# Performance work log

Hardware: AMD Instinct MI355X
Metric: run time of the kernel (lower is better)

## Reference

```python
import jax, jax.numpy as jnp
import numpy as np

N_WIRES = 10
DIM = 1 << N_WIRES          # 1024 amplitudes per token state
HIDDEN = 64                 # number of Pauli-Z-string measurements (= hidden_dim)
B, T = 8, 2048

# ops[k] = Z-string on qubits in bitmask (k+1): <psi|Z_mask|psi> = sum_i |psi_i|^2 * (-1)^popcount(i & mask)
_masks = np.arange(1, HIDDEN + 1, dtype=np.int64)
_ii = np.arange(DIM, dtype=np.int64)
_pc = (((_ii[None, :] & _masks[:, None])[..., None] >> np.arange(N_WIRES)) & 1).sum(-1)
SIGNS = jnp.asarray(1.0 - 2.0 * (_pc % 2), dtype=jnp.float32)   # (HIDDEN, DIM)

CNOT = jnp.array([[1, 0, 0, 0], [0, 1, 0, 0], [0, 0, 0, 1], [0, 0, 1, 0]], dtype=jnp.complex64)

def _rx(theta):
    c = jnp.cos(theta / 2).astype(jnp.complex64)
    s = jnp.sin(theta / 2).astype(jnp.complex64)
    return jnp.stack([jnp.stack([c, -1j * s]), jnp.stack([-1j * s, c])])

def _ry(theta):
    c = jnp.cos(theta / 2).astype(jnp.complex64)
    s = jnp.sin(theta / 2).astype(jnp.complex64)
    return jnp.stack([jnp.stack([c, -s]), jnp.stack([s, c])])

def _apply_1q(psi, g, j, n):
    # qubit 0 is the most-significant bit of the state index (matches expand_operator bit order)
    left, right = 1 << j, 1 << (n - 1 - j)
    p = psi.reshape(-1, left, 2, right)
    p = jnp.einsum('ab,mlbr->mlar', g, p)
    return p.reshape(-1, 1 << n)

def _apply_2q(psi, g, q0, q1, n):
    p = psi.reshape((-1,) + (2,) * n)
    p = jnp.moveaxis(p, (1 + q0, 1 + q1), (1, 2))
    p = jnp.einsum('abcd,mcd...->mab...', g.reshape(2, 2, 2, 2), p)
    p = jnp.moveaxis(p, (1, 2), (1 + q0, 1 + q1))
    return p.reshape(-1, 1 << n)

def _forward(x, rx0, ry0, ry1):
    n, dim = N_WIRES, DIM
    Bb, Tt, C = x.shape
    M = Bb * Tt
    # AmplitudeEncoder: zero-pad features to 2^n and L2-normalize
    psi = jnp.zeros((M, dim), jnp.complex64).at[:, :C].set(x.reshape(M, C).astype(jnp.complex64))
    nrm = jnp.sqrt(jnp.sum(psi.real**2 + psi.imag**2, axis=1, keepdims=True))
    psi = psi / nrm.astype(jnp.complex64)
    # U_total = (prod_j RY1_j) (prod_j CNOT_{j,(j+1)%n}) (prod_j RY0_j RX0_j), applied to psi.
    # Applying the gate sequence directly to the state == matmul with the expanded U_total.
    rx0_d = jax.lax.stop_gradient(rx0)  # original detaches RX params via .item()
    for j in range(n):
        psi = _apply_1q(psi, _rx(rx0_d[j]), j, n)
        psi = _apply_1q(psi, _ry(ry0[j]), j, n)
    for j in range(n):
        psi = _apply_2q(psi, CNOT, j, (j + 1) % n, n)
    for j in range(n):
        psi = _apply_1q(psi, _ry(ry1[j]), j, n)
    probs = psi.real**2 + psi.imag**2            # (M, DIM)
    out = probs @ SIGNS.T                        # (M, HIDDEN) Pauli-Z-string expectations
    return out.reshape(Bb, Tt, HIDDEN).astype(jnp.float32)

def setup_inputs():
    key = jax.random.key(0)
    k1, k2, k3, k4 = jax.random.split(key, 4)
    two_pi = 2.0 * float(np.pi)
    return {
        'x': jax.random.normal(k1, (B, T, HIDDEN), dtype=jnp.float32),
        'rx0': jax.random.uniform(k2, (N_WIRES,), dtype=jnp.float32, maxval=two_pi),
        'ry0': jax.random.uniform(k3, (N_WIRES,), dtype=jnp.float32, maxval=two_pi),
        'ry1': jax.random.uniform(k4, (N_WIRES,), dtype=jnp.float32, maxval=two_pi),
    }

def reference(x, rx0, ry0, ry1):
    return _forward(x, rx0, ry0, ry1)
```

## Files before the change

kernel.cpp:

```cpp
#include <hip/hip_runtime.h>

typedef __bf16 v8bf __attribute__((ext_vector_type(8)));
typedef float v4f __attribute__((ext_vector_type(4)));
typedef unsigned short u16x8 __attribute__((ext_vector_type(8)));

__device__ __forceinline__ unsigned short f2bf(float f) {
    unsigned int u = __float_as_uint(f);
    u += 0x7FFFu + ((u >> 16) & 1u);
    return (unsigned short)(u >> 16);
}

__device__ __forceinline__ v8bf ld_bf8(const unsigned short* p) {
    u16x8 r = *(const u16x8*)p;
    return __builtin_bit_cast(v8bf, r);
}

__device__ __forceinline__ float hw_cos(float h) {
    float r = h * 0.15915494309189535f, o;
    asm("v_cos_f32 %0, %1" : "=v"(o) : "v"(r));
    return o;
}
__device__ __forceinline__ float hw_sin(float h) {
    float r = h * 0.15915494309189535f, o;
    asm("v_sin_f32 %0, %1" : "=v"(o) : "v"(r));
    return o;
}

__global__ __launch_bounds__(64, 2) void build_V(
        const float* __restrict__ rx0, const float* __restrict__ ry0,
        const float* __restrict__ ry1,
        unsigned short* __restrict__ Vre, unsigned short* __restrict__ Vim)
{
    const int c = blockIdx.x;
    const int lane = threadIdx.x;

    float c1[10], s1[10];
    #pragma unroll
    for (int j = 0; j < 10; ++j) {
        float h = 0.5f * ry1[j];
        c1[j] = hw_cos(h); s1[j] = hw_sin(h);
    }

    int kk[16];
    #pragma unroll
    for (int q = 0; q < 16; ++q) {
        int k = lane + (q << 6);
        #pragma unroll
        for (int jj = 9; jj >= 0; --jj) {
            int cb = 9 - jj, tb = 9 - ((jj + 1) % 10);
            k ^= ((k >> cb) & 1) << tb;
        }
        kk[q] = k;
    }

    float ar[16], ai[16];
    #pragma unroll
    for (int q = 0; q < 16; ++q) { ar[q] = 1.f; ai[q] = 0.f; }

    #pragma unroll
    for (int j = 0; j < 10; ++j) {
        float hx = 0.5f * rx0[j], hy = 0.5f * ry0[j];
        float cx = hw_cos(hx), sx = hw_sin(hx), cy = hw_cos(hy), sy = hw_sin(hy);
        int cb = (c >> (9 - j)) & 1;
        float g0r = cb ? (-sy * cx) : (cy * cx);
        float g0i = cb ? (-cy * sx) : (sy * sx);
        float g1r = cb ? (cy * cx)  : (sy * cx);
        float g1i = cb ? (-sy * sx) : (-cy * sx);
        int p = 9 - j;
        #pragma unroll
        for (int q = 0; q < 16; ++q) {
            int kb = (kk[q] >> p) & 1;
            float fr = kb ? g1r : g0r;
            float fi = kb ? g1i : g0i;
            float nr = ar[q] * fr - ai[q] * fi;
            float ni = ar[q] * fi + ai[q] * fr;
            ar[q] = nr; ai[q] = ni;
        }
    }

    #pragma unroll
    for (int b = 0; b < 4; ++b) {
        float cy = c1[3 - b], sy = s1[3 - b];
        #pragma unroll
        for (int q = 0; q < 16; ++q) {
            if (q & (1 << b)) continue;
            int q2 = q | (1 << b);
            float A_r = ar[q], A_i = ai[q], B_r = ar[q2], B_i = ai[q2];
            ar[q]  = cy * A_r - sy * B_r;  ai[q]  = cy * A_i - sy * B_i;
            ar[q2] = sy * A_r + cy * B_r;  ai[q2] = sy * A_i + cy * B_i;
        }
    }
    #pragma unroll
    for (int p = 5; p >= 0; --p) {
        float cy = c1[9 - p], sy = s1[9 - p];
        int hi = (lane >> p) & 1;
        #pragma unroll
        for (int q = 0; q < 16; ++q) {
            float orr = __shfl_xor(ar[q], 1 << p);
            float oii = __shfl_xor(ai[q], 1 << p);
            ar[q] = hi ? (sy * orr + cy * ar[q]) : (cy * ar[q] - sy * orr);
            ai[q] = hi ? (sy * oii + cy * ai[q]) : (cy * ai[q] - sy * oii);
        }
    }

    #pragma unroll
    for (int q = 0; q < 16; ++q) {
        int i = lane + (q << 6);
        Vre[i * 64 + c] = f2bf(ar[q]);
        Vim[i * 64 + c] = f2bf(ai[q]);
    }
}

#define MFMA16(a, b, c) __builtin_amdgcn_mfma_f32_16x16x32_bf16(a, b, c, 0, 0, 0)

#define ISSUE(s, c) do {                                                     \
    _Pragma("unroll")                                                        \
    for (int _nb = 0; _nb < 4; ++_nb) {                                      \
        s[_nb*2+0] = ld_bf8(vb + (size_t)(c) * 4096 + _nb * 1024);           \
        s[_nb*2+1] = ld_bf8(vb + (size_t)(c) * 4096 + _nb * 1024 + 32);      \
    }                                                                        \
    __builtin_amdgcn_sched_barrier(0);                                       \
    } while (0)

#define COMP(s, q) do {                                                      \
    _Pragma("unroll")                                                        \
    for (int _nb = 0; _nb < 4; ++_nb) {                                      \
        v4f _z = (v4f){0.f, 0.f, 0.f, 0.f};                                  \
        v4f _r = MFMA16(a0, s[_nb*2+0], _z);                                 \
        _r     = MFMA16(a1, s[_nb*2+1], _r);                                 \
        _Pragma("unroll")                                                    \
        for (int _rr = 0; _rr < 4; ++_rr)                                    \
            q[_nb][_rr] += _r[_rr] * _r[_rr];                                \
    } } while (0)

#define GROUP(b) do {                                                        \
    if ((b) + 2 < 32) ISSUE(sC, (b) + 2);  COMP(sA, qE);                     \
    if ((b) + 3 < 32) ISSUE(sD, (b) + 3);  COMP(sB, qO);                     \
    if ((b) + 4 < 32) ISSUE(sA, (b) + 4);  COMP(sC, qE);                     \
    if ((b) + 5 < 32) ISSUE(sB, (b) + 5);  COMP(sD, qO);                     \
    } while (0)

__global__ __launch_bounds__(64) void qsa_fused(
        const float* __restrict__ x,
        const unsigned short* __restrict__ VS,
        float* __restrict__ out)
{
    const int l = threadIdx.x;
    const int l15 = l & 15, lh = l >> 4;
    const int tb = blockIdx.x * 16;

    const float* xrow = x + (size_t)(tb + l15) * 64;
    float4 v0 = *(const float4*)(xrow + lh * 8);
    float4 v1 = *(const float4*)(xrow + lh * 8 + 4);
    float4 v2 = *(const float4*)(xrow + 32 + lh * 8);
    float4 v3 = *(const float4*)(xrow + 32 + lh * 8 + 4);
    float ss = v0.x*v0.x + v0.y*v0.y + v0.z*v0.z + v0.w*v0.w
             + v1.x*v1.x + v1.y*v1.y + v1.z*v1.z + v1.w*v1.w
             + v2.x*v2.x + v2.y*v2.y + v2.z*v2.z + v2.w*v2.w
             + v3.x*v3.x + v3.y*v3.y + v3.z*v3.z + v3.w*v3.w;
    ss += __shfl_xor(ss, 16);
    ss += __shfl_xor(ss, 32);
    float rn = rsqrtf(ss);
    u16x8 ua0, ua1;
    ua0[0]=f2bf(v0.x*rn); ua0[1]=f2bf(v0.y*rn); ua0[2]=f2bf(v0.z*rn); ua0[3]=f2bf(v0.w*rn);
    ua0[4]=f2bf(v1.x*rn); ua0[5]=f2bf(v1.y*rn); ua0[6]=f2bf(v1.z*rn); ua0[7]=f2bf(v1.w*rn);
    ua1[0]=f2bf(v2.x*rn); ua1[1]=f2bf(v2.y*rn); ua1[2]=f2bf(v2.z*rn); ua1[3]=f2bf(v2.w*rn);
    ua1[4]=f2bf(v3.x*rn); ua1[5]=f2bf(v3.y*rn); ua1[6]=f2bf(v3.z*rn); ua1[7]=f2bf(v3.w*rn);
    const v8bf a0 = __builtin_bit_cast(v8bf, ua0);
    const v8bf a1 = __builtin_bit_cast(v8bf, ua1);

    const unsigned short* vb = VS + (size_t)l15 * 64 + lh * 8;

    float qE[4][4], qO[4][4];
    #pragma unroll
    for (int nb = 0; nb < 4; ++nb)
        #pragma unroll
        for (int rr = 0; rr < 4; ++rr) { qE[nb][rr] = 0.f; qO[nb][rr] = 0.f; }

    v8bf sA[8], sB[8], sC[8], sD[8];

    ISSUE(sA, 0);
    ISSUE(sB, 1);
    GROUP(0);  GROUP(4);  GROUP(8);  GROUP(12);
    GROUP(16); GROUP(20); GROUP(24); GROUP(28);

    #pragma unroll
    for (int rr = 0; rr < 4; ++rr) {
        float w8[8];
        #pragma unroll
        for (int nb = 0; nb < 4; ++nb) { w8[nb] = qE[nb][rr]; w8[4 + nb] = qO[nb][rr]; }

        #pragma unroll
        for (int i = 0; i < 4; ++i) {
            float u = w8[i], v = w8[i + 4];
            w8[i] = u + v; w8[i + 4] = u - v;
        }
        #pragma unroll
        for (int g = 0; g < 8; g += 4)
            #pragma unroll
            for (int i = 0; i < 2; ++i) {
                float u = w8[g + i], v = w8[g + i + 2];
                w8[g + i] = u + v; w8[g + i + 2] = u - v;
            }
        #pragma unroll
        for (int g = 0; g < 8; g += 2) {
            float u = w8[g], v = w8[g + 1];
            w8[g] = u + v; w8[g + 1] = u - v;
        }
        #pragma unroll
        for (int st = 1; st <= 8; st <<= 1) {
            #pragma unroll
            for (int k = 0; k < 8; ++k) {
                float o = __shfl_xor(w8[k], st);
                w8[k] = (l15 & st) ? (o - w8[k]) : (w8[k] + o);
            }
        }
        float* orow = out + (size_t)(tb + lh * 4 + rr) * 64;
        #pragma unroll
        for (int nb = 0; nb < 4; ++nb)
            if (nb != 0 || l15 != 0) orow[nb * 16 + l15 - 1] = w8[nb];
        if (l15 == 0) orow[63] = w8[4];
    }
}

extern "C" void kernel_launch(void* const* d_in, const int* in_sizes, int n_in,
                              void* d_out, int out_size, void* d_ws, size_t ws_size,
                              hipStream_t stream) {
    const float* x   = (const float*)d_in[0];
    const float* rx0 = (const float*)d_in[1];
    const float* ry0 = (const float*)d_in[2];
    const float* ry1 = (const float*)d_in[3];
    float* out = (float*)d_out;

    unsigned short* Vre = (unsigned short*)d_ws;
    unsigned short* Vim = Vre + 1024 * 64;

    const int M = in_sizes[0] / 64;

    build_V<<<64, 64, 0, stream>>>(rx0, ry0, ry1, Vre, Vim);
    qsa_fused<<<M / 16, 64, 0, stream>>>(x, Vre, out);
}
```

Baseline: 106.9 us.

## Split V chunk loop across two waves per block with LDS reduction

Each block now runs two wavefronts that each process half of the 32 V chunks (16 each), rather than one wave walking all 32. The second wave writes its partial squared accumulators to shared memory, and after a barrier the first wave adds them and performs the Walsh-Hadamard output transform. The software pipeline drops from four staging buffers to two to lower register use per wave. This roughly halves the serial MFMA and load chain per token tile and adds more waves per block, at the cost of an LDS round trip, a barrier, and the second wave sitting idle during the epilogue.

```diff
diff --git a/kernel.cpp b/kernel.cpp
--- a/kernel.cpp
+++ b/kernel.cpp
@@ -116,8 +116,8 @@
 #define ISSUE(s, c) do {                                                     \
     _Pragma("unroll")                                                        \
     for (int _nb = 0; _nb < 4; ++_nb) {                                      \
-        s[_nb*2+0] = ld_bf8(vb + (size_t)(c) * 4096 + _nb * 1024);           \
-        s[_nb*2+1] = ld_bf8(vb + (size_t)(c) * 4096 + _nb * 1024 + 32);      \
+        s[_nb*2+0] = ld_bf8(vbh + (size_t)(c) * 4096 + _nb * 1024);          \
+        s[_nb*2+1] = ld_bf8(vbh + (size_t)(c) * 4096 + _nb * 1024 + 32);     \
     }                                                                        \
     __builtin_amdgcn_sched_barrier(0);                                       \
     } while (0)
@@ -133,19 +133,21 @@
             q[_nb][_rr] += _r[_rr] * _r[_rr];                                \
     } } while (0)
 
-#define GROUP(b) do {                                                        \
-    if ((b) + 2 < 32) ISSUE(sC, (b) + 2);  COMP(sA, qE);                     \
-    if ((b) + 3 < 32) ISSUE(sD, (b) + 3);  COMP(sB, qO);                     \
-    if ((b) + 4 < 32) ISSUE(sA, (b) + 4);  COMP(sC, qE);                     \
-    if ((b) + 5 < 32) ISSUE(sB, (b) + 5);  COMP(sD, qO);                     \
+#define GR(b) do {                                                           \
+    if ((b) + 1 < 16) ISSUE(sB, (b) + 1);  COMP(sA, qE);                     \
+    if ((b) + 2 < 16) ISSUE(sA, (b) + 2);  COMP(sB, qO);                     \
     } while (0)
 
-__global__ __launch_bounds__(64) void qsa_fused(
+__global__ __launch_bounds__(128, 2) void qsa_fused(
         const float* __restrict__ x,
         const unsigned short* __restrict__ VS,
         float* __restrict__ out)
 {
-    const int l = threadIdx.x;
+    __shared__ float part[64][33];
+
+    const int tid = threadIdx.x;
+    const int w = tid >> 6;
+    const int l = tid & 63;
     const int l15 = l & 15, lh = l >> 4;
     const int tb = blockIdx.x * 16;
 
@@ -169,7 +171,7 @@
     const v8bf a0 = __builtin_bit_cast(v8bf, ua0);
     const v8bf a1 = __builtin_bit_cast(v8bf, ua1);
 
-    const unsigned short* vb = VS + (size_t)l15 * 64 + lh * 8;
+    const unsigned short* vbh = VS + (size_t)w * 16 * 4096 + (size_t)l15 * 64 + lh * 8;
 
     float qE[4][4], qO[4][4];
     #pragma unroll
@@ -177,49 +179,67 @@
         #pragma unroll
         for (int rr = 0; rr < 4; ++rr) { qE[nb][rr] = 0.f; qO[nb][rr] = 0.f; }
 
-    v8bf sA[8], sB[8], sC[8], sD[8];
+    v8bf sA[8], sB[8];
 
     ISSUE(sA, 0);
-    ISSUE(sB, 1);
-    GROUP(0);  GROUP(4);  GROUP(8);  GROUP(12);
-    GROUP(16); GROUP(20); GROUP(24); GROUP(28);
-
-    #pragma unroll
-    for (int rr = 0; rr < 4; ++rr) {
-        float w8[8];
-        #pragma unroll
-        for (int nb = 0; nb < 4; ++nb) { w8[nb] = qE[nb][rr]; w8[4 + nb] = qO[nb][rr]; }
-
-        #pragma unroll
-        for (int i = 0; i < 4; ++i) {
-            float u = w8[i], v = w8[i + 4];
-            w8[i] = u + v; w8[i + 4] = u - v;
-        }
-        #pragma unroll
-        for (int g = 0; g < 8; g += 4)
-            #pragma unroll
-            for (int i = 0; i < 2; ++i) {
-                float u = w8[g + i], v = w8[g + i + 2];
-                w8[g + i] = u + v; w8[g + i + 2] = u - v;
-            }
-        #pragma unroll
-        for (int g = 0; g < 8; g += 2) {
-            float u = w8[g], v = w8[g + 1];
-            w8[g] = u + v; w8[g + 1] = u - v;
-        }
-        #pragma unroll
-        for (int st = 1; st <= 8; st <<= 1) {
-            #pragma unroll
-            for (int k = 0; k < 8; ++k) {
-                float o = __shfl_xor(w8[k], st);
-                w8[k] = (l15 & st) ? (o - w8[k]) : (w8[k] + o);
-            }
-        }
-        float* orow = out + (size_t)(tb + lh * 4 + rr) * 64;
+    GR(0); GR(2); GR(4); GR(6); GR(8); GR(10); GR(12); GR(14);
+
+    if (w == 1) {
         #pragma unroll
         for (int nb = 0; nb < 4; ++nb)
-            if (nb != 0 || l15 != 0) orow[nb * 16 + l15 - 1] = w8[nb];
-        if (l15 == 0) orow[63] = w8[4];
+            #pragma unroll
+            for (int rr = 0; rr < 4; ++rr) {
+                part[l][nb * 4 + rr]      = qE[nb][rr];
+                part[l][16 + nb * 4 + rr] = qO[nb][rr];
+            }
+    }
+    __syncthreads();
+    if (w == 0) {
+        #pragma unroll
+        for (int nb = 0; nb < 4; ++nb)
+            #pragma unroll
+            for (int rr = 0; rr < 4; ++rr) {
+                qE[nb][rr] += part[l][nb * 4 + rr];
+                qO[nb][rr] += part[l][16 + nb * 4 + rr];
+            }
+
+        #pragma unroll
+        for (int rr = 0; rr < 4; ++rr) {
+            float w8[8];
+            #pragma unroll
+            for (int nb = 0; nb < 4; ++nb) { w8[nb] = qE[nb][rr]; w8[4 + nb] = qO[nb][rr]; }
+
+            #pragma unroll
+            for (int i = 0; i < 4; ++i) {
+                float u = w8[i], v = w8[i + 4];
+                w8[i] = u + v; w8[i + 4] = u - v;
+            }
+            #pragma unroll
+            for (int g = 0; g < 8; g += 4)
+                #pragma unroll
+                for (int i = 0; i < 2; ++i) {
+                    float u = w8[g + i], v = w8[g + i + 2];
+                    w8[g + i] = u + v; w8[g + i + 2] = u - v;
+                }
+            #pragma unroll
+            for (int g = 0; g < 8; g += 2) {
+                float u = w8[g], v = w8[g + 1];
+                w8[g] = u + v; w8[g + 1] = u - v;
+            }
+            #pragma unroll
+            for (int st = 1; st <= 8; st <<= 1) {
+                #pragma unroll
+                for (int k = 0; k < 8; ++k) {
+                    float o = __shfl_xor(w8[k], st);
+                    w8[k] = (l15 & st) ? (o - w8[k]) : (w8[k] + o);
+                }
+            }
+            float* orow = out + (size_t)(tb + lh * 4 + rr) * 64;
+            #pragma unroll
+            for (int nb = 0; nb < 4; ++nb)
+                if (nb != 0 || l15 != 0) orow[nb * 16 + l15 - 1] = w8[nb];
+            if (l15 == 0) orow[63] = w8[4];
+        }
     }
 }
 
@@ -238,5 +258,5 @@
     const int M = in_sizes[0] / 64;
 
     build_V<<<64, 64, 0, stream>>>(rx0, ry0, ry1, Vre, Vim);
-    qsa_fused<<<M / 16, 64, 0, stream>>>(x, Vre, out);
-}
+    qsa_fused<<<M / 16, 128, 0, stream>>>(x, Vre, out);
+}
```

Result: slower. 111.1 us (+4.0%).

## Use two-wave blocks with double buffering and pointer-increment loads

Applied to the files above, without the earlier changes.

Blocks now hold two waves of 64 threads, each handling its own 16 tokens, with launch bounds asking for 3 blocks per CU. The four-deep register prefetch ring (sA..sD) is cut to two buffers, and per-chunk address arithmetic is replaced by a running pointer. The goal is to free registers so more waves fit per CU and so latency is hidden by occupancy rather than deep prefetch. In exchange, each wave has less load lookahead of its own, which could expose memory latency if occupancy does not rise enough.

```diff
diff --git a/kernel.cpp b/kernel.cpp
--- a/kernel.cpp
+++ b/kernel.cpp
@@ -113,12 +113,14 @@
 
 #define MFMA16(a, b, c) __builtin_amdgcn_mfma_f32_16x16x32_bf16(a, b, c, 0, 0, 0)
 
-#define ISSUE(s, c) do {                                                     \
-    _Pragma("unroll")                                                        \
-    for (int _nb = 0; _nb < 4; ++_nb) {                                      \
-        s[_nb*2+0] = ld_bf8(vb + (size_t)(c) * 4096 + _nb * 1024);           \
-        s[_nb*2+1] = ld_bf8(vb + (size_t)(c) * 4096 + _nb * 1024 + 32);      \
-    }                                                                        \
+#define ISSUE(s) do {                                                        \
+    const unsigned short* _b0 = vp;                                          \
+    const unsigned short* _b1 = vp + 2048;                                   \
+    s[0] = ld_bf8(_b0);        s[1] = ld_bf8(_b0 + 32);                      \
+    s[2] = ld_bf8(_b0 + 1024); s[3] = ld_bf8(_b0 + 1056);                    \
+    s[4] = ld_bf8(_b1);        s[5] = ld_bf8(_b1 + 32);                      \
+    s[6] = ld_bf8(_b1 + 1024); s[7] = ld_bf8(_b1 + 1056);                    \
+    vp += 4096;                                                              \
     __builtin_amdgcn_sched_barrier(0);                                       \
     } while (0)
 
@@ -133,21 +135,18 @@
             q[_nb][_rr] += _r[_rr] * _r[_rr];                                \
     } } while (0)
 
-#define GROUP(b) do {                                                        \
-    if ((b) + 2 < 32) ISSUE(sC, (b) + 2);  COMP(sA, qE);                     \
-    if ((b) + 3 < 32) ISSUE(sD, (b) + 3);  COMP(sB, qO);                     \
-    if ((b) + 4 < 32) ISSUE(sA, (b) + 4);  COMP(sC, qE);                     \
-    if ((b) + 5 < 32) ISSUE(sB, (b) + 5);  COMP(sD, qO);                     \
-    } while (0)
-
-__global__ __launch_bounds__(64) void qsa_fused(
+#define STEP2 do { ISSUE(sB); COMP(sA, qE); ISSUE(sA); COMP(sB, qO); } while (0)
+
+__global__ __launch_bounds__(128, 3) void qsa_fused(
         const float* __restrict__ x,
         const unsigned short* __restrict__ VS,
         float* __restrict__ out)
 {
-    const int l = threadIdx.x;
+    const int tid = threadIdx.x;
+    const int w = tid >> 6;
+    const int l = tid & 63;
     const int l15 = l & 15, lh = l >> 4;
-    const int tb = blockIdx.x * 16;
+    const int tb = blockIdx.x * 32 + w * 16;
 
     const float* xrow = x + (size_t)(tb + l15) * 64;
     float4 v0 = *(const float4*)(xrow + lh * 8);
@@ -169,7 +168,7 @@
     const v8bf a0 = __builtin_bit_cast(v8bf, ua0);
     const v8bf a1 = __builtin_bit_cast(v8bf, ua1);
 
-    const unsigned short* vb = VS + (size_t)l15 * 64 + lh * 8;
+    const unsigned short* vp = VS + (size_t)l15 * 64 + lh * 8;
 
     float qE[4][4], qO[4][4];
     #pragma unroll
@@ -177,12 +176,15 @@
         #pragma unroll
         for (int rr = 0; rr < 4; ++rr) { qE[nb][rr] = 0.f; qO[nb][rr] = 0.f; }
 
-    v8bf sA[8], sB[8], sC[8], sD[8];
-
-    ISSUE(sA, 0);
-    ISSUE(sB, 1);
-    GROUP(0);  GROUP(4);  GROUP(8);  GROUP(12);
-    GROUP(16); GROUP(20); GROUP(24); GROUP(28);
+    v8bf sA[8], sB[8];
+
+    ISSUE(sA);
+    STEP2; STEP2; STEP2; STEP2; STEP2;
+    STEP2; STEP2; STEP2; STEP2; STEP2;
+    STEP2; STEP2; STEP2; STEP2; STEP2;
+    ISSUE(sB);
+    COMP(sA, qE);
+    COMP(sB, qO);
 
     #pragma unroll
     for (int rr = 0; rr < 4; ++rr) {
@@ -238,5 +240,5 @@
     const int M = in_sizes[0] / 64;
 
     build_V<<<64, 64, 0, stream>>>(rx0, ry0, ry1, Vre, Vim);
-    qsa_fused<<<M / 16, 64, 0, stream>>>(x, Vre, out);
-}
+    qsa_fused<<<M / 32, 128, 0, stream>>>(x, Vre, out);
+}
```

New measurement: 184.7 us. +72.8%, slower.
